# Performance work log

Hardware: AMD Instinct MI355X
Metric: run time of the kernel (lower is better)

## Reference

```python
import jax, jax.numpy as jnp
import numpy as np

N_NODES = 50000
N_EDGES = 1600000
D = 128


def setup_inputs() -> dict:
    key = jax.random.key(0)
    k1, k2, k3, k4 = jax.random.split(key, 4)
    x = jax.random.normal(k1, (N_NODES, D), dtype=jnp.float32)
    edge_index = jax.random.randint(k2, (2, N_EDGES), 0, N_NODES, dtype=jnp.int64)
    # Xavier-uniform-like W; B is zeros in torch init but use small random for grad coverage
    limit = float(np.sqrt(6.0 / (D + D)))
    W = jax.random.uniform(k3, (D, D), dtype=jnp.float32, minval=-limit, maxval=limit)
    B = jax.random.uniform(k4, (D, D), dtype=jnp.float32, minval=-limit, maxval=limit)
    return {"x": x, "edge_index": edge_index, "W": W, "B": B}


def reference(x, edge_index, W, B):
    sources = edge_index[0]
    destinations = edge_index[1]
    # gather messages from source nodes, scatter-add into destinations
    messages = x[sources]  # [E, D]
    aggregated = jax.ops.segment_sum(messages, destinations, num_segments=N_NODES)  # [N, D]
    deg = jax.ops.segment_sum(jnp.ones((N_EDGES,), dtype=x.dtype), destinations, num_segments=N_NODES)
    deg = jnp.where(deg == 0, jnp.asarray(1.0, dtype=x.dtype), deg)
    mean_msg = aggregated / deg[:, None]
    # update: messages @ W.T + x @ B.T
    return mean_msg @ W.T + x @ B.T
```

## Files before the change

kernel.cpp:

```cpp
#include <hip/hip_runtime.h>
#include <hip/hip_bf16.h>

#define NN 50000
#define NE 1600000
#define DD 128
#define NPB 64
#define NBK 782
#define MAXB 2560
#define CHUNK 3072
#define NCB 521
#define WS 136

typedef __attribute__((ext_vector_type(8))) short short8;
typedef __attribute__((ext_vector_type(4))) float f32x4;

__device__ inline unsigned short to_bf16(float v) {
    __hip_bfloat16 h = __float2bfloat16(v);
    return __builtin_bit_cast(unsigned short, h);
}
__device__ inline float bf2f(unsigned short u) {
    return __uint_as_float((unsigned)u << 16);
}

__global__ __launch_bounds__(1024) void convscatter_k(const int* __restrict__ ei,
                                                      const float* __restrict__ x,
                                                      const float* __restrict__ W,
                                                      const float* __restrict__ Bm,
                                                      unsigned int* __restrict__ xb,
                                                      unsigned short* __restrict__ Wbf,
                                                      unsigned short* __restrict__ Bbf,
                                                      int* __restrict__ gcursor,
                                                      int* __restrict__ ebuf) {
    __shared__ int stg[CHUNK];
    __shared__ int h[NBK];
    __shared__ int lbase[NBK];
    __shared__ int gb[NBK];
    __shared__ int hcur[NBK];
    __shared__ int wsum[16], wbase[16];
    const int t = threadIdx.x;
    const int lane = t & 63, wv = t >> 6;
    const int e0 = blockIdx.x * CHUNK;
    const int ec = min(CHUNK, NE - e0);

    for (int i = t; i < NBK; i += 1024) h[i] = 0;
    __syncthreads();

    unsigned int w2[3];
    #pragma unroll
    for (int u = 0; u < 3; ++u) {
        int i = u * 1024 + t;
        if (i < ec) {
            int src = ei[e0 + i];
            int dst = ei[NE + e0 + i];
            int b = dst >> 6;
            w2[u] = ((unsigned)b << 22) | ((unsigned)src << 6) | (unsigned)(dst & 63);
            atomicAdd(&h[b], 1);
        } else w2[u] = 0xFFFFFFFFu;
    }

    {
        int gid = blockIdx.x * 1024 + t;
        const int total4 = NN * DD / 4;
        for (int i = gid; i < total4; i += NCB * 1024) {
            float4 v = ((const float4*)x)[i];
            int p = __builtin_amdgcn_cvt_pk_fp8_f32(v.x, v.y, 0, false);
            p = __builtin_amdgcn_cvt_pk_fp8_f32(v.z, v.w, p, true);
            xb[i] = (unsigned)p;
        }
    }
    if (blockIdx.x == NCB - 1) {
        for (int i = t; i < DD * DD / 4; i += 1024) {
            float4 w4 = ((const float4*)W)[i];
            float4 b4 = ((const float4*)Bm)[i];
            ushort4 wp, bp;
            wp.x = to_bf16(w4.x); wp.y = to_bf16(w4.y); wp.z = to_bf16(w4.z); wp.w = to_bf16(w4.w);
            bp.x = to_bf16(b4.x); bp.y = to_bf16(b4.y); bp.z = to_bf16(b4.z); bp.w = to_bf16(b4.w);
            ((ushort4*)Wbf)[i] = wp;
            ((ushort4*)Bbf)[i] = bp;
        }
    }
    __syncthreads();

    int v = (t < NBK) ? h[t] : 0;
    int s = v;
    #pragma unroll
    for (int o = 1; o < 64; o <<= 1) {
        int u = __shfl_up(s, o);
        if (lane >= o) s += u;
    }
    if (lane == 63) wsum[wv] = s;
    __syncthreads();
    if (wv == 0 && lane < 16) {
        int bv = wsum[lane];
        int bs = bv;
        #pragma unroll
        for (int o = 1; o < 16; o <<= 1) {
            int u = __shfl_up(bs, o);
            if (lane >= o) bs += u;
        }
        wbase[lane] = bs - bv;
    }
    __syncthreads();
    if (t < NBK) {
        int excl = s - v + wbase[wv];
        lbase[t] = excl;
        hcur[t] = excl;
        gb[t] = v ? t * MAXB + atomicAdd(&gcursor[t], v) : 0;
    }
    __syncthreads();

    #pragma unroll
    for (int u = 0; u < 3; ++u) {
        if (w2[u] != 0xFFFFFFFFu) {
            int b = w2[u] >> 22;
            int pos = atomicAdd(&hcur[b], 1);
            stg[pos] = (int)w2[u];
        }
    }
    __syncthreads();

    for (int i = t; i < ec; i += 1024) {
        unsigned int w = (unsigned)stg[i];
        int b = w >> 22;
        ebuf[gb[b] + (i - lbase[b])] = (int)(w & 0x3FFFFFu);
    }
}

#define ACC2(U)                                                              \
    {                                                                        \
        auto l0 = __builtin_amdgcn_cvt_pk_f32_fp8((int)(U).x, false);        \
        auto h0 = __builtin_amdgcn_cvt_pk_f32_fp8((int)(U).x, true);         \
        auto l1 = __builtin_amdgcn_cvt_pk_f32_fp8((int)(U).y, false);        \
        auto h1 = __builtin_amdgcn_cvt_pk_f32_fp8((int)(U).y, true);         \
        a0 += l0[0]; a1 += l0[1]; a2 += h0[0]; a3 += h0[1];                  \
        a4 += l1[0]; a5 += l1[1]; a6 += h1[0]; a7 += h1[1];                  \
    }

__global__ __launch_bounds__(1024) void sortagg_k(const unsigned int* __restrict__ xb,
                                                  const int* __restrict__ ebuf,
                                                  const int* __restrict__ gcursor,
                                                  unsigned short* __restrict__ psb,
                                                  unsigned short* __restrict__ pcnt) {
    __shared__ int stg[MAXB];
    __shared__ unsigned short srt[MAXB];
    __shared__ int cnt16[16][NPB];
    __shared__ int cur[NPB], off[NPB + 1];
    const int b = blockIdx.x, t = threadIdx.x;
    const int wv = t >> 6, lane = t & 63;
    const int n = min(gcursor[b], MAXB);
    const int* __restrict__ slab = ebuf + (size_t)b * MAXB;

    cnt16[wv][lane] = 0;
    for (int i = t; i < n; i += 1024) {
        int v = slab[i];
        stg[i] = v;
        atomicAdd(&cnt16[wv][v & 63], 1);
    }
    __syncthreads();
    if (t < 64) {
        int v = 0;
        #pragma unroll
        for (int w = 0; w < 16; ++w) v += cnt16[w][t];
        int s = v;
        #pragma unroll
        for (int o = 1; o < 64; o <<= 1) {
            int u = __shfl_up(s, o);
            if (t >= o) s += u;
        }
        cur[t] = s - v;
        off[t] = s - v;
        if (t == 63) off[64] = s;
    }
    __syncthreads();
    for (int i = t; i < n; i += 1024) {
        int w = stg[i];
        int pos = atomicAdd(&cur[w & 63], 1);
        srt[pos] = (unsigned short)(w >> 6);
    }
    __syncthreads();

    const int sub = lane >> 4, il2 = lane & 15;
    #pragma unroll
    for (int q = 0; q < 4; ++q) {
        int ln = wv + q * 16;
        int s0 = off[ln], s1 = off[ln + 1];
        float a0 = 0.f, a1 = 0.f, a2 = 0.f, a3 = 0.f;
        float a4 = 0.f, a5 = 0.f, a6 = 0.f, a7 = 0.f;
        int i = s0;
        for (; i + 16 <= s1; i += 16) {
            uint2 u[4];
            #pragma unroll
            for (int k = 0; k < 4; ++k)
                u[k] = ((const uint2*)xb)[(size_t)srt[i + 4 * k + sub] * 16 + il2];
            #pragma unroll
            for (int k = 0; k < 4; ++k) ACC2(u[k]);
        }
        if (i < s1) {
            uint2 u[4];
            #pragma unroll
            for (int k = 0; k < 4; ++k) {
                int e = i + 4 * k + sub;
                if (e < s1) u[k] = ((const uint2*)xb)[(size_t)srt[e] * 16 + il2];
                else { u[k].x = 0u; u[k].y = 0u; }
            }
            #pragma unroll
            for (int k = 0; k < 4; ++k) ACC2(u[k]);
        }
        a0 += __shfl_xor(a0, 16); a0 += __shfl_xor(a0, 32);
        a1 += __shfl_xor(a1, 16); a1 += __shfl_xor(a1, 32);
        a2 += __shfl_xor(a2, 16); a2 += __shfl_xor(a2, 32);
        a3 += __shfl_xor(a3, 16); a3 += __shfl_xor(a3, 32);
        a4 += __shfl_xor(a4, 16); a4 += __shfl_xor(a4, 32);
        a5 += __shfl_xor(a5, 16); a5 += __shfl_xor(a5, 32);
        a6 += __shfl_xor(a6, 16); a6 += __shfl_xor(a6, 32);
        a7 += __shfl_xor(a7, 16); a7 += __shfl_xor(a7, 32);
        int node = b * NPB + ln;
        if (node < NN) {
            if (lane < 16) {
                short8 sv;
                sv[0] = (short)to_bf16(a0); sv[1] = (short)to_bf16(a1);
                sv[2] = (short)to_bf16(a2); sv[3] = (short)to_bf16(a3);
                sv[4] = (short)to_bf16(a4); sv[5] = (short)to_bf16(a5);
                sv[6] = (short)to_bf16(a6); sv[7] = (short)to_bf16(a7);
                *(short8*)&psb[(size_t)node * DD + il2 * 8] = sv;
            }
            if (lane == 0) pcnt[node] = (unsigned short)(s1 - s0);
        }
    }
}

__global__ __launch_bounds__(512) void gemm_mfma_k(const unsigned short* __restrict__ psb,
                                                   const unsigned short* __restrict__ pcnt,
                                                   const float* __restrict__ x,
                                                   const unsigned short* __restrict__ Wbf,
                                                   const unsigned short* __restrict__ Bbf,
                                                   float* __restrict__ out) {
    __shared__ unsigned short Wt[DD * WS];
    __shared__ unsigned short Bt[DD * WS];
    const int tid = threadIdx.x;
    #pragma unroll
    for (int it = 0; it < 8; ++it) {
        int idx = it * 512 + tid;
        int n = idx >> 5;
        int k0 = (idx & 31) * 4;
        *(ushort4*)&Wt[n * WS + k0] = ((const ushort4*)Wbf)[idx];
        *(ushort4*)&Bt[n * WS + k0] = ((const ushort4*)Bbf)[idx];
    }
    __syncthreads();

    const int wave = tid >> 6;
    const int lane = tid & 63;
    const int m = lane & 15;
    const int quad = lane >> 4;
    const int rowA = min(blockIdx.x * 128 + wave * 16 + m, NN - 1);

    const float deg = (float)pcnt[rowA];
    const float inv = 1.0f / fmaxf(deg, 1.0f);

    f32x4 acc[8];
    #pragma unroll
    for (int nt = 0; nt < 8; ++nt) acc[nt] = (f32x4){0.f, 0.f, 0.f, 0.f};

    #pragma unroll
    for (int t = 0; t < 4; ++t) {
        const int k8 = t * 32 + quad * 8;
        short8 p0 = *(const short8*)&psb[(size_t)rowA * DD + k8];
        short8 mf;
        #pragma unroll
        for (int j = 0; j < 8; ++j)
            mf[j] = (short)to_bf16(bf2f((unsigned short)p0[j]) * inv);

        float xv[8];
        {
            const float4* xq = (const float4*)&x[(size_t)rowA * DD + k8];
            float4 b0 = xq[0], b1 = xq[1];
            xv[0] = b0.x; xv[1] = b0.y; xv[2] = b0.z; xv[3] = b0.w;
            xv[4] = b1.x; xv[5] = b1.y; xv[6] = b1.z; xv[7] = b1.w;
        }
        short8 xh, xl;
        #pragma unroll
        for (int j = 0; j < 8; ++j) {
            unsigned short g = to_bf16(xv[j]);
            xh[j] = (short)g;
            xl[j] = (short)to_bf16(xv[j] - __uint_as_float((unsigned)g << 16));
        }
        #pragma unroll
        for (int nt = 0; nt < 8; ++nt) {
            int nrow = nt * 16 + m;
            short8 wf = *(const short8*)&Wt[nrow * WS + k8];
            short8 bf = *(const short8*)&Bt[nrow * WS + k8];
            acc[nt] = __builtin_amdgcn_mfma_f32_16x16x32_bf16(xl, bf, acc[nt], 0, 0, 0);
            acc[nt] = __builtin_amdgcn_mfma_f32_16x16x32_bf16(mf, wf, acc[nt], 0, 0, 0);
            acc[nt] = __builtin_amdgcn_mfma_f32_16x16x32_bf16(xh, bf, acc[nt], 0, 0, 0);
        }
    }

    const int rowD0 = blockIdx.x * 128 + wave * 16 + quad * 4;
    #pragma unroll
    for (int nt = 0; nt < 8; ++nt) {
        #pragma unroll
        for (int r = 0; r < 4; ++r) {
            int row = rowD0 + r;
            if (row < NN) out[(size_t)row * DD + nt * 16 + m] = acc[nt][r];
        }
    }
}

extern "C" void kernel_launch(void* const* d_in, const int* in_sizes, int n_in,
                              void* d_out, int out_size, void* d_ws, size_t ws_size,
                              hipStream_t stream) {
    const float* x  = (const float*)d_in[0];
    const int*   ei = (const int*)d_in[1];
    const float* W  = (const float*)d_in[2];
    const float* Bm = (const float*)d_in[3];
    float* out = (float*)d_out;

    unsigned short* psb  = (unsigned short*)d_ws;
    unsigned int* xb     = (unsigned int*)(psb + (size_t)NN * DD);
    int* ebuf            = (int*)(xb + (size_t)NN * 32);
    unsigned short* Wbf  = (unsigned short*)(ebuf + (size_t)NBK * MAXB);
    unsigned short* Bbf  = Wbf + DD * DD;
    unsigned short* pcnt = Bbf + DD * DD;
    int* gcursor         = (int*)(pcnt + (size_t)NN + (NN & 1));

    hipMemsetAsync(gcursor, 0, NBK * sizeof(int), stream);
    convscatter_k<<<NCB, 1024, 0, stream>>>(ei, x, W, Bm, xb, Wbf, Bbf, gcursor, ebuf);
    sortagg_k<<<NBK, 1024, 0, stream>>>(xb, ebuf, gcursor, psb, pcnt);
    gemm_mfma_k<<<(NN + 127) / 128, 512, 0, stream>>>(psb, pcnt, x, Wbf, Bbf, out);
}
```

Before: 154.4 us.

## Fuse three kernels into one persistent kernel with grid barriers and work queues

```diff
diff --git a/kernel.cpp b/kernel.cpp
--- a/kernel.cpp
+++ b/kernel.cpp
@@ -7,8 +7,11 @@
 #define NPB 64
 #define NBK 782
 #define MAXB 2560
-#define CHUNK 3072
-#define NCB 521
+#define GRID 448
+#define BLK 512
+#define CHUNK 3572
+#define NCH 448
+#define NT 391
 #define WS 136
 
 typedef __attribute__((ext_vector_type(8))) short short8;
@@ -22,108 +25,16 @@
     return __uint_as_float((unsigned)u << 16);
 }
 
-__global__ __launch_bounds__(1024) void convscatter_k(const int* __restrict__ ei,
-                                                      const float* __restrict__ x,
-                                                      const float* __restrict__ W,
-                                                      const float* __restrict__ Bm,
-                                                      unsigned int* __restrict__ xb,
-                                                      unsigned short* __restrict__ Wbf,
-                                                      unsigned short* __restrict__ Bbf,
-                                                      int* __restrict__ gcursor,
-                                                      int* __restrict__ ebuf) {
-    __shared__ int stg[CHUNK];
-    __shared__ int h[NBK];
-    __shared__ int lbase[NBK];
-    __shared__ int gb[NBK];
-    __shared__ int hcur[NBK];
-    __shared__ int wsum[16], wbase[16];
-    const int t = threadIdx.x;
-    const int lane = t & 63, wv = t >> 6;
-    const int e0 = blockIdx.x * CHUNK;
-    const int ec = min(CHUNK, NE - e0);
-
-    for (int i = t; i < NBK; i += 1024) h[i] = 0;
+__device__ inline void gridbar(int* bar, int target) {
     __syncthreads();
-
-    unsigned int w2[3];
-    #pragma unroll
-    for (int u = 0; u < 3; ++u) {
-        int i = u * 1024 + t;
-        if (i < ec) {
-            int src = ei[e0 + i];
-            int dst = ei[NE + e0 + i];
-            int b = dst >> 6;
-            w2[u] = ((unsigned)b << 22) | ((unsigned)src << 6) | (unsigned)(dst & 63);
-            atomicAdd(&h[b], 1);
-        } else w2[u] = 0xFFFFFFFFu;
-    }
-
-    {
-        int gid = blockIdx.x * 1024 + t;
-        const int total4 = NN * DD / 4;
-        for (int i = gid; i < total4; i += NCB * 1024) {
-            float4 v = ((const float4*)x)[i];
-            int p = __builtin_amdgcn_cvt_pk_fp8_f32(v.x, v.y, 0, false);
-            p = __builtin_amdgcn_cvt_pk_fp8_f32(v.z, v.w, p, true);
-            xb[i] = (unsigned)p;
-        }
-    }
-    if (blockIdx.x == NCB - 1) {
-        for (int i = t; i < DD * DD / 4; i += 1024) {
-            float4 w4 = ((const float4*)W)[i];
-            float4 b4 = ((const float4*)Bm)[i];
-            ushort4 wp, bp;
-            wp.x = to_bf16(w4.x); wp.y = to_bf16(w4.y); wp.z = to_bf16(w4.z); wp.w = to_bf16(w4.w);
-            bp.x = to_bf16(b4.x); bp.y = to_bf16(b4.y); bp.z = to_bf16(b4.z); bp.w = to_bf16(b4.w);
-            ((ushort4*)Wbf)[i] = wp;
-            ((ushort4*)Bbf)[i] = bp;
-        }
+    if (threadIdx.x == 0) {
+        __threadfence();
+        __hip_atomic_fetch_add(bar, 1, __ATOMIC_ACQ_REL, __HIP_MEMORY_SCOPE_AGENT);
+        while (__hip_atomic_load(bar, __ATOMIC_ACQUIRE, __HIP_MEMORY_SCOPE_AGENT) < target)
+            __builtin_amdgcn_s_sleep(8);
+        __threadfence();
     }
     __syncthreads();
-
-    int v = (t < NBK) ? h[t] : 0;
-    int s = v;
-    #pragma unroll
-    for (int o = 1; o < 64; o <<= 1) {
-        int u = __shfl_up(s, o);
-        if (lane >= o) s += u;
-    }
-    if (lane == 63) wsum[wv] = s;
-    __syncthreads();
-    if (wv == 0 && lane < 16) {
-        int bv = wsum[lane];
-        int bs = bv;
-        #pragma unroll
-        for (int o = 1; o < 16; o <<= 1) {
-            int u = __shfl_up(bs, o);
-            if (lane >= o) bs += u;
-        }
-        wbase[lane] = bs - bv;
-    }
-    __syncthreads();
-    if (t < NBK) {
-        int excl = s - v + wbase[wv];
-        lbase[t] = excl;
-        hcur[t] = excl;
-        gb[t] = v ? t * MAXB + atomicAdd(&gcursor[t], v) : 0;
-    }
-    __syncthreads();
-
-    #pragma unroll
-    for (int u = 0; u < 3; ++u) {
-        if (w2[u] != 0xFFFFFFFFu) {
-            int b = w2[u] >> 22;
-            int pos = atomicAdd(&hcur[b], 1);
-            stg[pos] = (int)w2[u];
-        }
-    }
-    __syncthreads();
-
-    for (int i = t; i < ec; i += 1024) {
-        unsigned int w = (unsigned)stg[i];
-        int b = w >> 22;
-        ebuf[gb[b] + (i - lbase[b])] = (int)(w & 0x3FFFFFu);
-    }
 }
 
 #define ACC2(U)                                                              \
@@ -136,172 +47,257 @@
         a4 += l1[0]; a5 += l1[1]; a6 += h1[0]; a7 += h1[1];                  \
     }
 
-__global__ __launch_bounds__(1024) void sortagg_k(const unsigned int* __restrict__ xb,
-                                                  const int* __restrict__ ebuf,
-                                                  const int* __restrict__ gcursor,
-                                                  unsigned short* __restrict__ psb,
-                                                  unsigned short* __restrict__ pcnt) {
-    __shared__ int stg[MAXB];
-    __shared__ unsigned short srt[MAXB];
-    __shared__ int cnt16[16][NPB];
-    __shared__ int cur[NPB], off[NPB + 1];
-    const int b = blockIdx.x, t = threadIdx.x;
-    const int wv = t >> 6, lane = t & 63;
-    const int n = min(gcursor[b], MAXB);
-    const int* __restrict__ slab = ebuf + (size_t)b * MAXB;
-
-    cnt16[wv][lane] = 0;
-    for (int i = t; i < n; i += 1024) {
-        int v = slab[i];
-        stg[i] = v;
-        atomicAdd(&cnt16[wv][v & 63], 1);
-    }
-    __syncthreads();
-    if (t < 64) {
-        int v = 0;
+__global__ __launch_bounds__(BLK, 4) void mega_k(
+        const int* __restrict__ ei, const float* __restrict__ x,
+        const float* __restrict__ W, const float* __restrict__ Bm,
+        int* __restrict__ ctl, unsigned int* __restrict__ xb,
+        int* __restrict__ ebuf, unsigned short* __restrict__ psb,
+        unsigned short* __restrict__ pcnt, float* __restrict__ out) {
+    __shared__ __align__(16) unsigned char lds[69632];
+    __shared__ int sh_id;
+    const int t = threadIdx.x, lane = t & 63, wv = t >> 6;
+    int* gcursor = ctl + 4;
+
+    {
+        const int total4 = NN * DD / 4;
+        for (int i = blockIdx.x * BLK + t; i < total4; i += GRID * BLK) {
+            float4 v = ((const float4*)x)[i];
+            int p = __builtin_amdgcn_cvt_pk_fp8_f32(v.x, v.y, 0, false);
+            p = __builtin_amdgcn_cvt_pk_fp8_f32(v.z, v.w, p, true);
+            xb[i] = (unsigned)p;
+        }
+    }
+
+    {
+        int* c_stg = (int*)lds;
+        int* c_h   = c_stg + 3584;
+        int* c_lb  = c_h + NBK;
+        int* c_gb  = c_lb + NBK;
+        int* c_hc  = c_gb + NBK;
+        int* c_ws  = c_hc + NBK;
+        int* c_wb  = c_ws + 8;
+        for (;;) {
+            if (t == 0) sh_id = atomicAdd(&ctl[1], 1);
+            __syncthreads();
+            const int c = sh_id;
+            if (c >= NCH) break;
+            const int e0 = c * CHUNK;
+            const int ec = min(CHUNK, NE - e0);
+            for (int i = t; i < NBK; i += BLK) c_h[i] = 0;
+            __syncthreads();
+            unsigned int w2[7];
+            #pragma unroll
+            for (int u = 0; u < 7; ++u) {
+                int i = u * BLK + t;
+                if (i < ec) {
+                    int src = ei[e0 + i], dst = ei[NE + e0 + i];
+                    int b = dst >> 6;
+                    w2[u] = ((unsigned)b << 22) | ((unsigned)src << 6) | (unsigned)(dst & 63);
+                    atomicAdd(&c_h[b], 1);
+                } else w2[u] = 0xFFFFFFFFu;
+            }
+            __syncthreads();
+            int va = 0, vb = 0, pv = 0;
+            if (t < 391) { va = c_h[2 * t]; vb = c_h[2 * t + 1]; pv = va + vb; }
+            int s = pv;
+            #pragma unroll
+            for (int o = 1; o < 64; o <<= 1) { int u = __shfl_up(s, o); if (lane >= o) s += u; }
+            if (lane == 63) c_ws[wv] = s;
+            __syncthreads();
+            if (wv == 0 && lane < 8) {
+                int bv = c_ws[lane], bs = bv;
+                #pragma unroll
+                for (int o = 1; o < 8; o <<= 1) { int u = __shfl_up(bs, o); if (lane >= o) bs += u; }
+                c_wb[lane] = bs - bv;
+            }
+            __syncthreads();
+            if (t < 391) {
+                int excl = s - pv + c_wb[wv];
+                c_lb[2 * t] = excl;          c_hc[2 * t] = excl;
+                c_lb[2 * t + 1] = excl + va; c_hc[2 * t + 1] = excl + va;
+                c_gb[2 * t]     = va ? (2 * t) * MAXB     + atomicAdd(&gcursor[2 * t], va)     : 0;
+                c_gb[2 * t + 1] = vb ? (2 * t + 1) * MAXB + atomicAdd(&gcursor[2 * t + 1], vb) : 0;
+            }
+            __syncthreads();
+            #pragma unroll
+            for (int u = 0; u < 7; ++u) {
+                if (w2[u] != 0xFFFFFFFFu) {
+                    int b = w2[u] >> 22;
+                    int pos = atomicAdd(&c_hc[b], 1);
+                    c_stg[pos] = (int)w2[u];
+                }
+            }
+            __syncthreads();
+            for (int i = t; i < ec; i += BLK) {
+                unsigned int w = (unsigned)c_stg[i];
+                int b = w >> 22;
+                ebuf[c_gb[b] + (i - c_lb[b])] = (int)(w & 0x3FFFFFu);
+            }
+            __syncthreads();
+        }
+    }
+    gridbar(&ctl[0], GRID);
+
+    {
+        int* a_stg = (int*)lds;
+        unsigned short* a_srt = (unsigned short*)(lds + MAXB * 4);
+        int* a_c8  = (int*)(lds + MAXB * 6);
+        int* a_cur = a_c8 + 8 * 64;
+        int* a_off = a_cur + 64;
+        const int sub = lane >> 4, il2 = lane & 15;
+        for (;;) {
+            if (t == 0) sh_id = atomicAdd(&ctl[2], 1);
+            __syncthreads();
+            const int b = sh_id;
+            if (b >= NBK) break;
+            const int n = min(gcursor[b], MAXB);
+            const int* __restrict__ slab = ebuf + (size_t)b * MAXB;
+            a_c8[wv * 64 + lane] = 0;
+            for (int i = t; i < n; i += BLK) {
+                int v = slab[i];
+                a_stg[i] = v;
+                atomicAdd(&a_c8[wv * 64 + (v & 63)], 1);
+            }
+            __syncthreads();
+            if (t < 64) {
+                int v = 0;
+                #pragma unroll
+                for (int w = 0; w < 8; ++w) v += a_c8[w * 64 + t];
+                int s2 = v;
+                #pragma unroll
+                for (int o = 1; o < 64; o <<= 1) { int u = __shfl_up(s2, o); if (t >= o) s2 += u; }
+                a_cur[t] = s2 - v; a_off[t] = s2 - v;
+                if (t == 63) a_off[64] = s2;
+            }
+            __syncthreads();
+            for (int i = t; i < n; i += BLK) {
+                int w = a_stg[i];
+                int pos = atomicAdd(&a_cur[w & 63], 1);
+                a_srt[pos] = (unsigned short)(w >> 6);
+            }
+            __syncthreads();
+            #pragma unroll
+            for (int q = 0; q < 8; ++q) {
+                int ln = wv + q * 8;
+                int s0 = a_off[ln], s1 = a_off[ln + 1];
+                float a0 = 0.f, a1 = 0.f, a2 = 0.f, a3 = 0.f;
+                float a4 = 0.f, a5 = 0.f, a6 = 0.f, a7 = 0.f;
+                int i = s0;
+                for (; i + 16 <= s1; i += 16) {
+                    uint2 u[4];
+                    #pragma unroll
+                    for (int k = 0; k < 4; ++k)
+                        u[k] = ((const uint2*)xb)[(size_t)a_srt[i + 4 * k + sub] * 16 + il2];
+                    #pragma unroll
+                    for (int k = 0; k < 4; ++k) ACC2(u[k]);
+                }
+                if (i < s1) {
+                    uint2 u[4];
+                    #pragma unroll
+                    for (int k = 0; k < 4; ++k) {
+                        int e = i + 4 * k + sub;
+                        if (e < s1) u[k] = ((const uint2*)xb)[(size_t)a_srt[e] * 16 + il2];
+                        else { u[k].x = 0u; u[k].y = 0u; }
+                    }
+                    #pragma unroll
+                    for (int k = 0; k < 4; ++k) ACC2(u[k]);
+                }
+                a0 += __shfl_xor(a0, 16); a0 += __shfl_xor(a0, 32);
+                a1 += __shfl_xor(a1, 16); a1 += __shfl_xor(a1, 32);
+                a2 += __shfl_xor(a2, 16); a2 += __shfl_xor(a2, 32);
+                a3 += __shfl_xor(a3, 16); a3 += __shfl_xor(a3, 32);
+                a4 += __shfl_xor(a4, 16); a4 += __shfl_xor(a4, 32);
+                a5 += __shfl_xor(a5, 16); a5 += __shfl_xor(a5, 32);
+                a6 += __shfl_xor(a6, 16); a6 += __shfl_xor(a6, 32);
+                a7 += __shfl_xor(a7, 16); a7 += __shfl_xor(a7, 32);
+                int node = b * NPB + ln;
+                if (node < NN) {
+                    if (lane < 16) {
+                        short8 sv;
+                        sv[0] = (short)to_bf16(a0); sv[1] = (short)to_bf16(a1);
+                        sv[2] = (short)to_bf16(a2); sv[3] = (short)to_bf16(a3);
+                        sv[4] = (short)to_bf16(a4); sv[5] = (short)to_bf16(a5);
+                        sv[6] = (short)to_bf16(a6); sv[7] = (short)to_bf16(a7);
+                        *(short8*)&psb[(size_t)node * DD + il2 * 8] = sv;
+                    }
+                    if (lane == 0) pcnt[node] = (unsigned short)(s1 - s0);
+                }
+            }
+            __syncthreads();
+        }
+    }
+    gridbar(&ctl[0], 2 * GRID);
+
+    {
+        unsigned short* Wt = (unsigned short*)lds;
+        unsigned short* Bt = Wt + DD * WS;
         #pragma unroll
-        for (int w = 0; w < 16; ++w) v += cnt16[w][t];
-        int s = v;
-        #pragma unroll
-        for (int o = 1; o < 64; o <<= 1) {
-            int u = __shfl_up(s, o);
-            if (t >= o) s += u;
-        }
-        cur[t] = s - v;
-        off[t] = s - v;
-        if (t == 63) off[64] = s;
-    }
-    __syncthreads();
-    for (int i = t; i < n; i += 1024) {
-        int w = stg[i];
-        int pos = atomicAdd(&cur[w & 63], 1);
-        srt[pos] = (unsigned short)(w >> 6);
-    }
-    __syncthreads();
-
-    const int sub = lane >> 4, il2 = lane & 15;
-    #pragma unroll
-    for (int q = 0; q < 4; ++q) {
-        int ln = wv + q * 16;
-        int s0 = off[ln], s1 = off[ln + 1];
-        float a0 = 0.f, a1 = 0.f, a2 = 0.f, a3 = 0.f;
-        float a4 = 0.f, a5 = 0.f, a6 = 0.f, a7 = 0.f;
-        int i = s0;
-        for (; i + 16 <= s1; i += 16) {
-            uint2 u[4];
-            #pragma unroll
-            for (int k = 0; k < 4; ++k)
-                u[k] = ((const uint2*)xb)[(size_t)srt[i + 4 * k + sub] * 16 + il2];
-            #pragma unroll
-            for (int k = 0; k < 4; ++k) ACC2(u[k]);
-        }
-        if (i < s1) {
-            uint2 u[4];
-            #pragma unroll
-            for (int k = 0; k < 4; ++k) {
-                int e = i + 4 * k + sub;
-                if (e < s1) u[k] = ((const uint2*)xb)[(size_t)srt[e] * 16 + il2];
-                else { u[k].x = 0u; u[k].y = 0u; }
-            }
-            #pragma unroll
-            for (int k = 0; k < 4; ++k) ACC2(u[k]);
-        }
-        a0 += __shfl_xor(a0, 16); a0 += __shfl_xor(a0, 32);
-        a1 += __shfl_xor(a1, 16); a1 += __shfl_xor(a1, 32);
-        a2 += __shfl_xor(a2, 16); a2 += __shfl_xor(a2, 32);
-        a3 += __shfl_xor(a3, 16); a3 += __shfl_xor(a3, 32);
-        a4 += __shfl_xor(a4, 16); a4 += __shfl_xor(a4, 32);
-        a5 += __shfl_xor(a5, 16); a5 += __shfl_xor(a5, 32);
-        a6 += __shfl_xor(a6, 16); a6 += __shfl_xor(a6, 32);
-        a7 += __shfl_xor(a7, 16); a7 += __shfl_xor(a7, 32);
-        int node = b * NPB + ln;
-        if (node < NN) {
-            if (lane < 16) {
-                short8 sv;
-                sv[0] = (short)to_bf16(a0); sv[1] = (short)to_bf16(a1);
-                sv[2] = (short)to_bf16(a2); sv[3] = (short)to_bf16(a3);
-                sv[4] = (short)to_bf16(a4); sv[5] = (short)to_bf16(a5);
-                sv[6] = (short)to_bf16(a6); sv[7] = (short)to_bf16(a7);
-                *(short8*)&psb[(size_t)node * DD + il2 * 8] = sv;
-            }
-            if (lane == 0) pcnt[node] = (unsigned short)(s1 - s0);
-        }
-    }
-}
-
-__global__ __launch_bounds__(512) void gemm_mfma_k(const unsigned short* __restrict__ psb,
-                                                   const unsigned short* __restrict__ pcnt,
-                                                   const float* __restrict__ x,
-                                                   const unsigned short* __restrict__ Wbf,
-                                                   const unsigned short* __restrict__ Bbf,
-                                                   float* __restrict__ out) {
-    __shared__ unsigned short Wt[DD * WS];
-    __shared__ unsigned short Bt[DD * WS];
-    const int tid = threadIdx.x;
-    #pragma unroll
-    for (int it = 0; it < 8; ++it) {
-        int idx = it * 512 + tid;
-        int n = idx >> 5;
-        int k0 = (idx & 31) * 4;
-        *(ushort4*)&Wt[n * WS + k0] = ((const ushort4*)Wbf)[idx];
-        *(ushort4*)&Bt[n * WS + k0] = ((const ushort4*)Bbf)[idx];
-    }
-    __syncthreads();
-
-    const int wave = tid >> 6;
-    const int lane = tid & 63;
-    const int m = lane & 15;
-    const int quad = lane >> 4;
-    const int rowA = min(blockIdx.x * 128 + wave * 16 + m, NN - 1);
-
-    const float deg = (float)pcnt[rowA];
-    const float inv = 1.0f / fmaxf(deg, 1.0f);
-
-    f32x4 acc[8];
-    #pragma unroll
-    for (int nt = 0; nt < 8; ++nt) acc[nt] = (f32x4){0.f, 0.f, 0.f, 0.f};
-
-    #pragma unroll
-    for (int t = 0; t < 4; ++t) {
-        const int k8 = t * 32 + quad * 8;
-        short8 p0 = *(const short8*)&psb[(size_t)rowA * DD + k8];
-        short8 mf;
-        #pragma unroll
-        for (int j = 0; j < 8; ++j)
-            mf[j] = (short)to_bf16(bf2f((unsigned short)p0[j]) * inv);
-
-        float xv[8];
-        {
-            const float4* xq = (const float4*)&x[(size_t)rowA * DD + k8];
-            float4 b0 = xq[0], b1 = xq[1];
-            xv[0] = b0.x; xv[1] = b0.y; xv[2] = b0.z; xv[3] = b0.w;
-            xv[4] = b1.x; xv[5] = b1.y; xv[6] = b1.z; xv[7] = b1.w;
-        }
-        short8 xh, xl;
-        #pragma unroll
-        for (int j = 0; j < 8; ++j) {
-            unsigned short g = to_bf16(xv[j]);
-            xh[j] = (short)g;
-            xl[j] = (short)to_bf16(xv[j] - __uint_as_float((unsigned)g << 16));
-        }
-        #pragma unroll
-        for (int nt = 0; nt < 8; ++nt) {
-            int nrow = nt * 16 + m;
-            short8 wf = *(const short8*)&Wt[nrow * WS + k8];
-            short8 bf = *(const short8*)&Bt[nrow * WS + k8];
-            acc[nt] = __builtin_amdgcn_mfma_f32_16x16x32_bf16(xl, bf, acc[nt], 0, 0, 0);
-            acc[nt] = __builtin_amdgcn_mfma_f32_16x16x32_bf16(mf, wf, acc[nt], 0, 0, 0);
-            acc[nt] = __builtin_amdgcn_mfma_f32_16x16x32_bf16(xh, bf, acc[nt], 0, 0, 0);
-        }
-    }
-
-    const int rowD0 = blockIdx.x * 128 + wave * 16 + quad * 4;
-    #pragma unroll
-    for (int nt = 0; nt < 8; ++nt) {
-        #pragma unroll
-        for (int r = 0; r < 4; ++r) {
-            int row = rowD0 + r;
-            if (row < NN) out[(size_t)row * DD + nt * 16 + m] = acc[nt][r];
+        for (int it = 0; it < 8; ++it) {
+            int idx = it * BLK + t;
+            int nrow = idx >> 5, k0 = (idx & 31) * 4;
+            float4 w4 = ((const float4*)W)[idx];
+            float4 b4 = ((const float4*)Bm)[idx];
+            ushort4 wp, bp;
+            wp.x = to_bf16(w4.x); wp.y = to_bf16(w4.y); wp.z = to_bf16(w4.z); wp.w = to_bf16(w4.w);
+            bp.x = to_bf16(b4.x); bp.y = to_bf16(b4.y); bp.z = to_bf16(b4.z); bp.w = to_bf16(b4.w);
+            *(ushort4*)&Wt[nrow * WS + k0] = wp;
+            *(ushort4*)&Bt[nrow * WS + k0] = bp;
+        }
+        __syncthreads();
+        const int m = lane & 15, quad = lane >> 4;
+        for (;;) {
+            if (t == 0) sh_id = atomicAdd(&ctl[3], 1);
+            __syncthreads();
+            const int tile = sh_id;
+            if (tile >= NT) break;
+            const int rowA = min(tile * 128 + wv * 16 + m, NN - 1);
+            const float deg = (float)pcnt[rowA];
+            const float inv = 1.0f / fmaxf(deg, 1.0f);
+            f32x4 acc[8];
+            #pragma unroll
+            for (int nt = 0; nt < 8; ++nt) acc[nt] = (f32x4){0.f, 0.f, 0.f, 0.f};
+            #pragma unroll
+            for (int tt = 0; tt < 4; ++tt) {
+                const int k8 = tt * 32 + quad * 8;
+                short8 p0 = *(const short8*)&psb[(size_t)rowA * DD + k8];
+                short8 mf;
+                #pragma unroll
+                for (int j = 0; j < 8; ++j)
+                    mf[j] = (short)to_bf16(bf2f((unsigned short)p0[j]) * inv);
+                float xv[8];
+                {
+                    const float4* xq = (const float4*)&x[(size_t)rowA * DD + k8];
+                    float4 b0 = xq[0], b1 = xq[1];
+                    xv[0] = b0.x; xv[1] = b0.y; xv[2] = b0.z; xv[3] = b0.w;
+                    xv[4] = b1.x; xv[5] = b1.y; xv[6] = b1.z; xv[7] = b1.w;
+                }
+                short8 xh, xl;
+                #pragma unroll
+                for (int j = 0; j < 8; ++j) {
+                    unsigned short g = to_bf16(xv[j]);
+                    xh[j] = (short)g;
+                    xl[j] = (short)to_bf16(xv[j] - __uint_as_float((unsigned)g << 16));
+                }
+                #pragma unroll
+                for (int nt = 0; nt < 8; ++nt) {
+                    int nrow = nt * 16 + m;
+                    short8 wf = *(const short8*)&Wt[nrow * WS + k8];
+                    short8 bf = *(const short8*)&Bt[nrow * WS + k8];
+                    acc[nt] = __builtin_amdgcn_mfma_f32_16x16x32_bf16(xl, bf, acc[nt], 0, 0, 0);
+                    acc[nt] = __builtin_amdgcn_mfma_f32_16x16x32_bf16(mf, wf, acc[nt], 0, 0, 0);
+                    acc[nt] = __builtin_amdgcn_mfma_f32_16x16x32_bf16(xh, bf, acc[nt], 0, 0, 0);
+                }
+            }
+            const int rowD0 = tile * 128 + wv * 16 + quad * 4;
+            #pragma unroll
+            for (int nt = 0; nt < 8; ++nt) {
+                #pragma unroll
+                for (int r = 0; r < 4; ++r) {
+                    int row = rowD0 + r;
+                    if (row < NN) out[(size_t)row * DD + nt * 16 + m] = acc[nt][r];
+                }
+            }
+            __syncthreads();
         }
     }
 }
@@ -315,16 +311,12 @@
     const float* Bm = (const float*)d_in[3];
     float* out = (float*)d_out;
 
-    unsigned short* psb  = (unsigned short*)d_ws;
-    unsigned int* xb     = (unsigned int*)(psb + (size_t)NN * DD);
+    int* ctl             = (int*)d_ws;
+    unsigned int* xb     = (unsigned int*)d_ws + 1024;
     int* ebuf            = (int*)(xb + (size_t)NN * 32);
-    unsigned short* Wbf  = (unsigned short*)(ebuf + (size_t)NBK * MAXB);
-    unsigned short* Bbf  = Wbf + DD * DD;
-    unsigned short* pcnt = Bbf + DD * DD;
-    int* gcursor         = (int*)(pcnt + (size_t)NN + (NN & 1));
-
-    hipMemsetAsync(gcursor, 0, NBK * sizeof(int), stream);
-    convscatter_k<<<NCB, 1024, 0, stream>>>(ei, x, W, Bm, xb, Wbf, Bbf, gcursor, ebuf);
-    sortagg_k<<<NBK, 1024, 0, stream>>>(xb, ebuf, gcursor, psb, pcnt);
-    gemm_mfma_k<<<(NN + 127) / 128, 512, 0, stream>>>(psb, pcnt, x, Wbf, Bbf, out);
-}
+    unsigned short* psb  = (unsigned short*)(ebuf + (size_t)NBK * MAXB);
+    unsigned short* pcnt = psb + (size_t)NN * DD;
+
+    hipMemsetAsync(ctl, 0, (4 + NBK) * sizeof(int), stream);
+    mega_k<<<GRID, BLK, 0, stream>>>(ei, x, W, Bm, ctl, xb, ebuf, psb, pcnt, out);
+}
```

After: 383.3 us. 2.48x slower.

## Fuse aggregation and MFMA GEMM into one kernel via shared-memory means

Applied to the files above, without the earlier changes.

```diff
diff --git a/kernel.cpp b/kernel.cpp
--- a/kernel.cpp
+++ b/kernel.cpp
@@ -9,7 +9,7 @@
 #define MAXB 2560
 #define CHUNK 3072
 #define NCB 521
-#define WS 136
+#define MWS 136
 
 typedef __attribute__((ext_vector_type(8))) short short8;
 typedef __attribute__((ext_vector_type(4))) float f32x4;
@@ -17,9 +17,6 @@
 __device__ inline unsigned short to_bf16(float v) {
     __hip_bfloat16 h = __float2bfloat16(v);
     return __builtin_bit_cast(unsigned short, h);
-}
-__device__ inline float bf2f(unsigned short u) {
-    return __uint_as_float((unsigned)u << 16);
 }
 
 __global__ __launch_bounds__(1024) void convscatter_k(const int* __restrict__ ei,
@@ -136,15 +133,18 @@
         a4 += l1[0]; a5 += l1[1]; a6 += h1[0]; a7 += h1[1];                  \
     }
 
-__global__ __launch_bounds__(1024) void sortagg_k(const unsigned int* __restrict__ xb,
-                                                  const int* __restrict__ ebuf,
-                                                  const int* __restrict__ gcursor,
-                                                  unsigned short* __restrict__ psb,
-                                                  unsigned short* __restrict__ pcnt) {
+__global__ __launch_bounds__(1024, 8) void aggemm_k(const unsigned int* __restrict__ xb,
+                                                    const int* __restrict__ ebuf,
+                                                    const int* __restrict__ gcursor,
+                                                    const unsigned short* __restrict__ Wbf,
+                                                    const unsigned short* __restrict__ Bbf,
+                                                    const float* __restrict__ x,
+                                                    float* __restrict__ out) {
     __shared__ int stg[MAXB];
     __shared__ unsigned short srt[MAXB];
     __shared__ int cnt16[16][NPB];
     __shared__ int cur[NPB], off[NPB + 1];
+    __shared__ unsigned short meanL[NPB * MWS];
     const int b = blockIdx.x, t = threadIdx.x;
     const int wv = t >> 6, lane = t & 63;
     const int n = min(gcursor[b], MAXB);
@@ -214,62 +214,31 @@
         a5 += __shfl_xor(a5, 16); a5 += __shfl_xor(a5, 32);
         a6 += __shfl_xor(a6, 16); a6 += __shfl_xor(a6, 32);
         a7 += __shfl_xor(a7, 16); a7 += __shfl_xor(a7, 32);
-        int node = b * NPB + ln;
-        if (node < NN) {
-            if (lane < 16) {
-                short8 sv;
-                sv[0] = (short)to_bf16(a0); sv[1] = (short)to_bf16(a1);
-                sv[2] = (short)to_bf16(a2); sv[3] = (short)to_bf16(a3);
-                sv[4] = (short)to_bf16(a4); sv[5] = (short)to_bf16(a5);
-                sv[6] = (short)to_bf16(a6); sv[7] = (short)to_bf16(a7);
-                *(short8*)&psb[(size_t)node * DD + il2 * 8] = sv;
-            }
-            if (lane == 0) pcnt[node] = (unsigned short)(s1 - s0);
-        }
-    }
-}
-
-__global__ __launch_bounds__(512) void gemm_mfma_k(const unsigned short* __restrict__ psb,
-                                                   const unsigned short* __restrict__ pcnt,
-                                                   const float* __restrict__ x,
-                                                   const unsigned short* __restrict__ Wbf,
-                                                   const unsigned short* __restrict__ Bbf,
-                                                   float* __restrict__ out) {
-    __shared__ unsigned short Wt[DD * WS];
-    __shared__ unsigned short Bt[DD * WS];
-    const int tid = threadIdx.x;
-    #pragma unroll
-    for (int it = 0; it < 8; ++it) {
-        int idx = it * 512 + tid;
-        int n = idx >> 5;
-        int k0 = (idx & 31) * 4;
-        *(ushort4*)&Wt[n * WS + k0] = ((const ushort4*)Wbf)[idx];
-        *(ushort4*)&Bt[n * WS + k0] = ((const ushort4*)Bbf)[idx];
-    }
-    __syncthreads();
-
-    const int wave = tid >> 6;
-    const int lane = tid & 63;
-    const int m = lane & 15;
-    const int quad = lane >> 4;
-    const int rowA = min(blockIdx.x * 128 + wave * 16 + m, NN - 1);
-
-    const float deg = (float)pcnt[rowA];
-    const float inv = 1.0f / fmaxf(deg, 1.0f);
-
-    f32x4 acc[8];
-    #pragma unroll
-    for (int nt = 0; nt < 8; ++nt) acc[nt] = (f32x4){0.f, 0.f, 0.f, 0.f};
-
-    #pragma unroll
-    for (int t = 0; t < 4; ++t) {
-        const int k8 = t * 32 + quad * 8;
-        short8 p0 = *(const short8*)&psb[(size_t)rowA * DD + k8];
-        short8 mf;
-        #pragma unroll
-        for (int j = 0; j < 8; ++j)
-            mf[j] = (short)to_bf16(bf2f((unsigned short)p0[j]) * inv);
-
+        if (lane < 16) {
+            float inv = 1.0f / fmaxf((float)(s1 - s0), 1.0f);
+            short8 sv;
+            sv[0] = (short)to_bf16(a0 * inv); sv[1] = (short)to_bf16(a1 * inv);
+            sv[2] = (short)to_bf16(a2 * inv); sv[3] = (short)to_bf16(a3 * inv);
+            sv[4] = (short)to_bf16(a4 * inv); sv[5] = (short)to_bf16(a5 * inv);
+            sv[6] = (short)to_bf16(a6 * inv); sv[7] = (short)to_bf16(a7 * inv);
+            *(short8*)&meanL[ln * MWS + il2 * 8] = sv;
+        }
+    }
+    __syncthreads();
+
+    const int m = lane & 15, quad = lane >> 4;
+    const int rt = wv & 3, cg = wv >> 2;
+    const int rowLoc = rt * 16 + m;
+    const int rowA = min(b * 64 + rowLoc, NN - 1);
+
+    f32x4 acc[2];
+    acc[0] = (f32x4){0.f, 0.f, 0.f, 0.f};
+    acc[1] = (f32x4){0.f, 0.f, 0.f, 0.f};
+
+    #pragma unroll
+    for (int tt = 0; tt < 4; ++tt) {
+        const int k8 = tt * 32 + quad * 8;
+        short8 mf = *(const short8*)&meanL[rowLoc * MWS + k8];
         float xv[8];
         {
             const float4* xq = (const float4*)&x[(size_t)rowA * DD + k8];
@@ -285,23 +254,23 @@
             xl[j] = (short)to_bf16(xv[j] - __uint_as_float((unsigned)g << 16));
         }
         #pragma unroll
-        for (int nt = 0; nt < 8; ++nt) {
-            int nrow = nt * 16 + m;
-            short8 wf = *(const short8*)&Wt[nrow * WS + k8];
-            short8 bf = *(const short8*)&Bt[nrow * WS + k8];
-            acc[nt] = __builtin_amdgcn_mfma_f32_16x16x32_bf16(xl, bf, acc[nt], 0, 0, 0);
-            acc[nt] = __builtin_amdgcn_mfma_f32_16x16x32_bf16(mf, wf, acc[nt], 0, 0, 0);
-            acc[nt] = __builtin_amdgcn_mfma_f32_16x16x32_bf16(xh, bf, acc[nt], 0, 0, 0);
-        }
-    }
-
-    const int rowD0 = blockIdx.x * 128 + wave * 16 + quad * 4;
-    #pragma unroll
-    for (int nt = 0; nt < 8; ++nt) {
+        for (int j = 0; j < 2; ++j) {
+            int nrow = (cg * 2 + j) * 16 + m;
+            short8 wf = *(const short8*)&Wbf[(size_t)nrow * DD + k8];
+            short8 bf = *(const short8*)&Bbf[(size_t)nrow * DD + k8];
+            acc[j] = __builtin_amdgcn_mfma_f32_16x16x32_bf16(xl, bf, acc[j], 0, 0, 0);
+            acc[j] = __builtin_amdgcn_mfma_f32_16x16x32_bf16(mf, wf, acc[j], 0, 0, 0);
+            acc[j] = __builtin_amdgcn_mfma_f32_16x16x32_bf16(xh, bf, acc[j], 0, 0, 0);
+        }
+    }
+
+    const int rowD0 = b * 64 + rt * 16 + quad * 4;
+    #pragma unroll
+    for (int j = 0; j < 2; ++j) {
         #pragma unroll
         for (int r = 0; r < 4; ++r) {
             int row = rowD0 + r;
-            if (row < NN) out[(size_t)row * DD + nt * 16 + m] = acc[nt][r];
+            if (row < NN) out[(size_t)row * DD + (cg * 2 + j) * 16 + m] = acc[j][r];
         }
     }
 }
@@ -315,16 +284,13 @@
     const float* Bm = (const float*)d_in[3];
     float* out = (float*)d_out;
 
-    unsigned short* psb  = (unsigned short*)d_ws;
-    unsigned int* xb     = (unsigned int*)(psb + (size_t)NN * DD);
+    unsigned int* xb     = (unsigned int*)d_ws;
     int* ebuf            = (int*)(xb + (size_t)NN * 32);
     unsigned short* Wbf  = (unsigned short*)(ebuf + (size_t)NBK * MAXB);
     unsigned short* Bbf  = Wbf + DD * DD;
-    unsigned short* pcnt = Bbf + DD * DD;
-    int* gcursor         = (int*)(pcnt + (size_t)NN + (NN & 1));
+    int* gcursor         = (int*)(Bbf + DD * DD);
 
     hipMemsetAsync(gcursor, 0, NBK * sizeof(int), stream);
     convscatter_k<<<NCB, 1024, 0, stream>>>(ei, x, W, Bm, xb, Wbf, Bbf, gcursor, ebuf);
-    sortagg_k<<<NBK, 1024, 0, stream>>>(xb, ebuf, gcursor, psb, pcnt);
-    gemm_mfma_k<<<(NN + 127) / 128, 512, 0, stream>>>(psb, pcnt, x, Wbf, Bbf, out);
-}
+    aggemm_k<<<NBK, 1024, 0, stream>>>(xb, ebuf, gcursor, Wbf, Bbf, x, out);
+}
```

New measurement: 177.9 us. 1.15x slower.

## Replace global bucket atomics with per-chunk offset table and coalesced writes

Applied to the files above, without the earlier changes.

```diff
diff --git a/kernel.cpp b/kernel.cpp
--- a/kernel.cpp
+++ b/kernel.cpp
@@ -6,9 +6,10 @@
 #define DD 128
 #define NPB 64
 #define NBK 782
-#define MAXB 2560
+#define SMAX 3072
 #define CHUNK 3072
 #define NCB 521
+#define OTS 784
 #define WS 136
 
 typedef __attribute__((ext_vector_type(8))) short short8;
@@ -29,12 +30,11 @@
                                                       unsigned int* __restrict__ xb,
                                                       unsigned short* __restrict__ Wbf,
                                                       unsigned short* __restrict__ Bbf,
-                                                      int* __restrict__ gcursor,
-                                                      int* __restrict__ ebuf) {
+                                                      int* __restrict__ ebuf,
+                                                      unsigned short* __restrict__ offtab) {
     __shared__ int stg[CHUNK];
     __shared__ int h[NBK];
     __shared__ int lbase[NBK];
-    __shared__ int gb[NBK];
     __shared__ int hcur[NBK];
     __shared__ int wsum[16], wbase[16];
     const int t = threadIdx.x;
@@ -105,25 +105,24 @@
         int excl = s - v + wbase[wv];
         lbase[t] = excl;
         hcur[t] = excl;
-        gb[t] = v ? t * MAXB + atomicAdd(&gcursor[t], v) : 0;
-    }
-    __syncthreads();
+    }
+    __syncthreads();
+
+    for (int i = t; i <= NBK; i += 1024)
+        offtab[(size_t)blockIdx.x * OTS + i] = (unsigned short)((i < NBK) ? lbase[i] : ec);
 
     #pragma unroll
     for (int u = 0; u < 3; ++u) {
         if (w2[u] != 0xFFFFFFFFu) {
             int b = w2[u] >> 22;
             int pos = atomicAdd(&hcur[b], 1);
-            stg[pos] = (int)w2[u];
-        }
-    }
-    __syncthreads();
-
-    for (int i = t; i < ec; i += 1024) {
-        unsigned int w = (unsigned)stg[i];
-        int b = w >> 22;
-        ebuf[gb[b] + (i - lbase[b])] = (int)(w & 0x3FFFFFu);
-    }
+            stg[pos] = (int)(w2[u] & 0x3FFFFFu);
+        }
+    }
+    __syncthreads();
+
+    for (int i = t; i < (ec >> 2); i += 1024)
+        ((int4*)(ebuf + e0))[i] = ((const int4*)stg)[i];
 }
 
 #define ACC2(U)                                                              \
@@ -138,38 +137,77 @@
 
 __global__ __launch_bounds__(1024) void sortagg_k(const unsigned int* __restrict__ xb,
                                                   const int* __restrict__ ebuf,
-                                                  const int* __restrict__ gcursor,
+                                                  const unsigned short* __restrict__ offtab,
                                                   unsigned short* __restrict__ psb,
                                                   unsigned short* __restrict__ pcnt) {
-    __shared__ int stg[MAXB];
-    __shared__ unsigned short srt[MAXB];
+    __shared__ int stg[SMAX];
+    __shared__ unsigned short srt[SMAX];
     __shared__ int cnt16[16][NPB];
     __shared__ int cur[NPB], off[NPB + 1];
+    __shared__ int segoff[NCB + 1];
+    __shared__ int srcb[NCB];
+    __shared__ int ws16[16], wb16[16];
     const int b = blockIdx.x, t = threadIdx.x;
     const int wv = t >> 6, lane = t & 63;
-    const int n = min(gcursor[b], MAXB);
-    const int* __restrict__ slab = ebuf + (size_t)b * MAXB;
-
+
+    int v = 0;
+    if (t < NCB) {
+        int o1 = offtab[(size_t)t * OTS + b];
+        int o2 = offtab[(size_t)t * OTS + b + 1];
+        v = o2 - o1;
+        srcb[t] = t * CHUNK + o1;
+    }
+    int s = v;
+    #pragma unroll
+    for (int o = 1; o < 64; o <<= 1) {
+        int u = __shfl_up(s, o);
+        if (lane >= o) s += u;
+    }
+    if (lane == 63) ws16[wv] = s;
     cnt16[wv][lane] = 0;
+    __syncthreads();
+    if (wv == 0 && lane < 16) {
+        int bv = ws16[lane], bs = bv;
+        #pragma unroll
+        for (int o = 1; o < 16; o <<= 1) {
+            int u = __shfl_up(bs, o);
+            if (lane >= o) bs += u;
+        }
+        wb16[lane] = bs - bv;
+    }
+    __syncthreads();
+    int excl = s - v + wb16[wv];
+    if (t < NCB) segoff[t] = excl;
+    if (t == NCB - 1) segoff[NCB] = excl + v;
+    __syncthreads();
+    const int n = min(segoff[NCB], SMAX);
+
     for (int i = t; i < n; i += 1024) {
-        int v = slab[i];
-        stg[i] = v;
-        atomicAdd(&cnt16[wv][v & 63], 1);
-    }
-    __syncthreads();
+        int lo = 0, hi = NCB - 1;
+        #pragma unroll
+        for (int it = 0; it < 10; ++it) {
+            int mid = (lo + hi + 1) >> 1;
+            if (segoff[mid] <= i) lo = mid; else hi = mid - 1;
+        }
+        int val = ebuf[srcb[lo] + (i - segoff[lo])];
+        stg[i] = val;
+        atomicAdd(&cnt16[wv][val & 63], 1);
+    }
+    __syncthreads();
+
     if (t < 64) {
-        int v = 0;
-        #pragma unroll
-        for (int w = 0; w < 16; ++w) v += cnt16[w][t];
-        int s = v;
+        int vv = 0;
+        #pragma unroll
+        for (int w = 0; w < 16; ++w) vv += cnt16[w][t];
+        int ss = vv;
         #pragma unroll
         for (int o = 1; o < 64; o <<= 1) {
-            int u = __shfl_up(s, o);
-            if (t >= o) s += u;
-        }
-        cur[t] = s - v;
-        off[t] = s - v;
-        if (t == 63) off[64] = s;
+            int u = __shfl_up(ss, o);
+            if (t >= o) ss += u;
+        }
+        cur[t] = ss - vv;
+        off[t] = ss - vv;
+        if (t == 63) off[64] = ss;
     }
     __syncthreads();
     for (int i = t; i < n; i += 1024) {
@@ -315,16 +353,15 @@
     const float* Bm = (const float*)d_in[3];
     float* out = (float*)d_out;
 
-    unsigned short* psb  = (unsigned short*)d_ws;
-    unsigned int* xb     = (unsigned int*)(psb + (size_t)NN * DD);
-    int* ebuf            = (int*)(xb + (size_t)NN * 32);
-    unsigned short* Wbf  = (unsigned short*)(ebuf + (size_t)NBK * MAXB);
-    unsigned short* Bbf  = Wbf + DD * DD;
-    unsigned short* pcnt = Bbf + DD * DD;
-    int* gcursor         = (int*)(pcnt + (size_t)NN + (NN & 1));
-
-    hipMemsetAsync(gcursor, 0, NBK * sizeof(int), stream);
-    convscatter_k<<<NCB, 1024, 0, stream>>>(ei, x, W, Bm, xb, Wbf, Bbf, gcursor, ebuf);
-    sortagg_k<<<NBK, 1024, 0, stream>>>(xb, ebuf, gcursor, psb, pcnt);
+    unsigned int* xb      = (unsigned int*)d_ws;
+    int* ebuf             = (int*)(xb + (size_t)NN * 32);
+    unsigned short* offtab= (unsigned short*)(ebuf + (size_t)NE);
+    unsigned short* Wbf   = offtab + (size_t)NCB * OTS;
+    unsigned short* Bbf   = Wbf + DD * DD;
+    unsigned short* psb   = Bbf + DD * DD;
+    unsigned short* pcnt  = psb + (size_t)NN * DD;
+
+    convscatter_k<<<NCB, 1024, 0, stream>>>(ei, x, W, Bm, xb, Wbf, Bbf, ebuf, offtab);
+    sortagg_k<<<NBK, 1024, 0, stream>>>(xb, ebuf, offtab, psb, pcnt);
     gemm_mfma_k<<<(NN + 127) / 128, 512, 0, stream>>>(psb, pcnt, x, Wbf, Bbf, out);
 }
```

Measured after the change: 141.9 us. 1.09x faster.
